# Kernel optimization log

Hardware: AMD Instinct MI355X
Metric: run time of the kernel (lower is better)

Reference implementation:

```python
import jax, jax.numpy as jnp
import numpy as np

B, H, W, D, C = 2, 128, 128, 8, 64
HEADS, DIM_HEAD = 4, 16
F_IN = C * D            # 512
F_OUT = DIM_HEAD * HEADS * D  # 512


def setup_inputs() -> dict:
    key = jax.random.key(0)
    ks = jax.random.split(key, 8)
    s = 0.02
    return {
        "x_in": jax.random.normal(ks[0], (B, H, W, D, C), dtype=jnp.float32),
        "Wq": jax.random.normal(ks[1], (F_IN, F_OUT), dtype=jnp.float32) * s,
        "Wk": jax.random.normal(ks[2], (F_IN, F_OUT), dtype=jnp.float32) * s,
        "Wv": jax.random.normal(ks[3], (F_IN, F_OUT), dtype=jnp.float32) * s,
        "rescale": jnp.ones((HEADS, 1, 1), dtype=jnp.float32),
        "Wp": jax.random.normal(ks[4], (F_OUT, F_IN), dtype=jnp.float32) * s,
        "bp": jnp.zeros((F_IN,), dtype=jnp.float32),
        "pos_w1": jax.random.normal(ks[5], (C, 1, 3, 3, 3), dtype=jnp.float32) * s,
        "pos_w2": jax.random.normal(ks[6], (C, 1, 3, 3, 3), dtype=jnp.float32) * s,
    }


def _dwconv3d(y, kern, groups):
    # y: [b,c,d,h,w], kern: [c,1,3,3,3] depthwise
    return jax.lax.conv_general_dilated(
        y, kern, window_strides=(1, 1, 1), padding="SAME",
        feature_group_count=groups,
        dimension_numbers=("NCDHW", "OIDHW", "NCDHW"))


def reference(x_in, Wq, Wk, Wv, rescale, Wp, bp, pos_w1, pos_w2):
    b, h, w, d, c = x_in.shape
    heads = rescale.shape[0]
    n = h * w
    x = x_in.reshape(b, n, d * c)
    q_inp = x @ Wq
    k_inp = x @ Wk
    v_inp = x @ Wv

    def split(t):  # [b,n,heads*Dh] -> [b,heads,Dh,n]  (Dh = dim_head*num_frm)
        return t.reshape(b, n, heads, -1).transpose(0, 2, 3, 1)

    q, k, v = split(q_inp), split(k_inp), split(v_inp)
    # L2-normalize along spatial axis n (last dim), torch F.normalize eps=1e-12
    q = q / jnp.maximum(jnp.linalg.norm(q, axis=-1, keepdims=True), 1e-12)
    k = k / jnp.maximum(jnp.linalg.norm(k, axis=-1, keepdims=True), 1e-12)
    # channel attention: [b,heads,Dh,Dh]
    attn = jnp.einsum("bhdn,bhen->bhde", k, q) * rescale
    attn = jax.nn.softmax(attn, axis=-1)
    out = jnp.einsum("bhde,bhen->bhdn", attn, v)  # [b,heads,Dh,n]
    out = out.transpose(0, 3, 1, 2).reshape(b, n, -1)  # [b,n,heads*Dh]
    out_c = (out @ Wp + bp).reshape(b, h, w, d, c)

    # positional branch: depthwise conv3d over [b,c,d,h,w]
    vp = v_inp.reshape(b, h, w, d, c).transpose(0, 4, 3, 1, 2)
    p = _dwconv3d(vp, pos_w1, c)
    p = jax.nn.gelu(p, approximate=False)
    p = _dwconv3d(p, pos_w2, c)
    out_p = p.transpose(0, 3, 4, 2, 1)  # -> [b,h,w,d,c]
    return out_c + out_p
```

## Files before the change

### kernel.cpp

```cpp
#include <hip/hip_runtime.h>
#include <math.h>
#include <stdint.h>


using short8  = __attribute__((ext_vector_type(8))) short;
using short4v = __attribute__((ext_vector_type(4))) short;
using f32x4   = __attribute__((ext_vector_type(4))) float;

__device__ __forceinline__ float bf2f(unsigned short u) {
  union { unsigned int i; float f; } v; v.i = ((unsigned int)u) << 16; return v.f;
}
__device__ __forceinline__ unsigned short f2bf(float f) {
  union { float f; unsigned int i; } v; v.f = f;
  unsigned int r = v.i + 0x7fffu + ((v.i >> 16) & 1u);
  return (unsigned short)(r >> 16);
}

__device__ __forceinline__ void g2l16(const void* g, void* l) {
  __builtin_amdgcn_global_load_lds(
      (__attribute__((address_space(1))) void*)(unsigned long long)(uintptr_t)g,
      (__attribute__((address_space(3))) void*)(unsigned int)(uintptr_t)l,
      16, 0, 0);
}

__global__ __launch_bounds__(256) void convert_x(const float* __restrict__ x,
                                                 unsigned short* __restrict__ xb) {
  int i = (blockIdx.x * 256 + threadIdx.x) * 4;
  float4 v = *(const float4*)&x[i];
  ushort4 o;
  o.x = f2bf(v.x); o.y = f2bf(v.y); o.z = f2bf(v.z); o.w = f2bf(v.w);
  *(ushort4*)&xb[i] = o;
}

__global__ __launch_bounds__(256) void prep_w(const float* __restrict__ Wq,
                                              const float* __restrict__ Wk,
                                              const float* __restrict__ Wv,
                                              const float* __restrict__ Wp,
                                              unsigned short* __restrict__ Wcat_t,
                                              unsigned short* __restrict__ Wp_t) {
  __shared__ unsigned short Ls[32 * 36];
  int bid = blockIdx.x;
  int mat = bid >> 8, tile = bid & 255;
  int tr = (tile >> 4) * 32, tc = (tile & 15) * 32;
  const float* src = (mat == 0) ? Wq : (mat == 1) ? Wk : (mat == 2) ? Wv : Wp;
  int t = threadIdx.x;
  int r = t >> 3, c4 = (t & 7) * 4;
  float4 v = *(const float4*)&src[(tr + r) * 512 + tc + c4];
  Ls[(c4 + 0) * 36 + r] = f2bf(v.x);
  Ls[(c4 + 1) * 36 + r] = f2bf(v.y);
  Ls[(c4 + 2) * 36 + r] = f2bf(v.z);
  Ls[(c4 + 3) * 36 + r] = f2bf(v.w);
  __syncthreads();
  int rn = t >> 3, ck4 = (t & 7) * 4;
  ushort4 o;
  o.x = Ls[rn * 36 + ck4 + 0]; o.y = Ls[rn * 36 + ck4 + 1];
  o.z = Ls[rn * 36 + ck4 + 2]; o.w = Ls[rn * 36 + ck4 + 3];
  unsigned short* dst = (mat < 3)
      ? &Wcat_t[(long)(mat * 512 + tc + rn) * 512 + tr + ck4]
      : &Wp_t[(long)(tc + rn) * 512 + tr + ck4];
  *(ushort4*)dst = o;
}

__global__ __launch_bounds__(256) void gemm_lds(
    const unsigned short* __restrict__ A, const unsigned short* __restrict__ Bt,
    unsigned short* __restrict__ C, const float* __restrict__ bias,
    int lda, int ldb, int ldc, int K, long sA, long sB, long sC) {
  __shared__ unsigned short As[128 * 64];
  __shared__ unsigned short Bs[128 * 64];
  const int t = threadIdx.x;
  const int n0 = blockIdx.x * 128, m0 = blockIdx.y * 128;
  A  += (long)blockIdx.z * sA + (long)m0 * lda;
  Bt += (long)blockIdx.z * sB + (long)n0 * ldb;
  C  += (long)blockIdx.z * sC;
  const int lane = t & 63, w = t >> 6;
  const int wm = w >> 1, wn = w & 1;
  const int quad = lane >> 4, l16 = lane & 15;
  const int sr = lane >> 3;
  const int sc = lane & 7;

  f32x4 acc[4][4] = {};

  for (int k0 = 0; k0 < K; k0 += 64) {
#pragma unroll
    for (int q = 0; q < 4; q++) {
      int r = q * 32 + w * 8 + sr;
      int ca = (sc ^ sr) * 8;
      g2l16(&A[(long)r * lda + k0 + ca], &As[(q * 32 + w * 8) * 64]);
      g2l16(&Bt[(long)r * ldb + k0 + ca], &Bs[(q * 32 + w * 8) * 64]);
    }
    __syncthreads();
#pragma unroll
    for (int kk = 0; kk < 2; kk++) {
      short8 af[4], bfq[4];
#pragma unroll
      for (int i = 0; i < 4; i++) {
        int r = wm * 64 + i * 16 + l16;
        int s = (kk * 4 + quad) ^ (r & 7);
        af[i] = *(const short8*)&As[r * 64 + s * 8];
      }
#pragma unroll
      for (int j = 0; j < 4; j++) {
        int r = wn * 64 + j * 16 + l16;
        int s = (kk * 4 + quad) ^ (r & 7);
        bfq[j] = *(const short8*)&Bs[r * 64 + s * 8];
      }
#pragma unroll
      for (int i = 0; i < 4; i++)
#pragma unroll
        for (int j = 0; j < 4; j++)
          acc[i][j] = __builtin_amdgcn_mfma_f32_16x16x32_bf16(bfq[j], af[i], acc[i][j], 0, 0, 0);
    }
    __syncthreads();
  }

#pragma unroll
  for (int i = 0; i < 4; i++) {
    long rbase = (long)(m0 + wm * 64 + i * 16 + l16) * ldc;
#pragma unroll
    for (int j = 0; j < 4; j++) {
      int col = n0 + wn * 64 + j * 16 + quad * 4;
      float b0 = 0.f, b1 = 0.f, b2 = 0.f, b3 = 0.f;
      if (bias) { float4 bv = *(const float4*)&bias[col]; b0 = bv.x; b1 = bv.y; b2 = bv.z; b3 = bv.w; }
      uint2 o;
      o.x = (unsigned)f2bf(acc[i][j][0] + b0) | ((unsigned)f2bf(acc[i][j][1] + b1) << 16);
      o.y = (unsigned)f2bf(acc[i][j][2] + b2) | ((unsigned)f2bf(acc[i][j][3] + b3) << 16);
      *(uint2*)&C[rbase + col] = o;
    }
  }
}

__global__ __launch_bounds__(256) void gram_kernel(const unsigned short* __restrict__ qkv,
                                                   float* __restrict__ Gp,
                                                   float* __restrict__ ss) {
  __shared__ unsigned short Qs[128 * 36];
  __shared__ unsigned short Ks[128 * 36];
  int ns = blockIdx.x, h = blockIdx.y, b = blockIdx.z;
  int t = threadIdx.x;
  const int lane = t & 63, wave = t >> 6;
  const int wm = wave >> 1, wn = wave & 1;
  const int quad = lane >> 4, l16 = lane & 15;
  long base = (long)b * 16384 * 1536;
  int m = t >> 7;
  int tt = t & 127;
  int cg = tt & 31;
  int rg = tt >> 5;
  int colb = (m ? (512 + h * 128) : (h * 128)) + cg * 4;
  unsigned short* dst = m ? Ks : Qs;

  f32x4 acc[4][4] = {};
  float ssp[4] = {0.f, 0.f, 0.f, 0.f};

  for (int s = 0; s < 16; s++) {
    int n0 = ns * 512 + s * 32;
    unsigned short sv[8][4];
#pragma unroll
    for (int rr = 0; rr < 8; rr++) {
      int n = n0 + rg * 8 + rr;
      uint2 v = *(const uint2*)&qkv[base + (long)n * 1536 + colb];
      sv[rr][0] = (unsigned short)(v.x & 0xffff);
      sv[rr][1] = (unsigned short)(v.x >> 16);
      sv[rr][2] = (unsigned short)(v.y & 0xffff);
      sv[rr][3] = (unsigned short)(v.y >> 16);
    }
#pragma unroll
    for (int rr = 0; rr < 8; rr++)
#pragma unroll
      for (int j = 0; j < 4; j++) {
        float fv = bf2f(sv[rr][j]);
        ssp[j] += fv * fv;
      }
#pragma unroll
    for (int j = 0; j < 4; j++) {
      int col = cg * 4 + j;
      ushort4 w0 = { sv[0][j], sv[1][j], sv[2][j], sv[3][j] };
      ushort4 w1 = { sv[4][j], sv[5][j], sv[6][j], sv[7][j] };
      *(ushort4*)&dst[col * 36 + rg * 8]     = w0;
      *(ushort4*)&dst[col * 36 + rg * 8 + 4] = w1;
    }
    __syncthreads();
    short8 af[4], bfq[4];
#pragma unroll
    for (int i = 0; i < 4; i++) {
      const unsigned short* p = &Ks[(wm * 64 + i * 16 + l16) * 36 + quad * 8];
      union { short8 v8; short4v v4[2]; } u;
      u.v4[0] = *(const short4v*)p; u.v4[1] = *(const short4v*)(p + 4);
      af[i] = u.v8;
    }
#pragma unroll
    for (int j = 0; j < 4; j++) {
      const unsigned short* p = &Qs[(wn * 64 + j * 16 + l16) * 36 + quad * 8];
      union { short8 v8; short4v v4[2]; } u;
      u.v4[0] = *(const short4v*)p; u.v4[1] = *(const short4v*)(p + 4);
      bfq[j] = u.v8;
    }
#pragma unroll
    for (int i = 0; i < 4; i++)
#pragma unroll
      for (int j = 0; j < 4; j++)
        acc[i][j] = __builtin_amdgcn_mfma_f32_16x16x32_bf16(bfq[j], af[i], acc[i][j], 0, 0, 0);
    __syncthreads();
  }

  float* gp = Gp + ((long)ns * 8 + b * 4 + h) * 16384;
#pragma unroll
  for (int i = 0; i < 4; i++) {
    int row = wm * 64 + i * 16 + l16;
#pragma unroll
    for (int j = 0; j < 4; j++) {
      int col = wn * 64 + j * 16 + quad * 4;
      *(f32x4*)&gp[row * 128 + col] = acc[i][j];
    }
  }

  float* sred = (float*)Qs;
#pragma unroll
  for (int j = 0; j < 4; j++) sred[(m * 128 + cg * 4 + j) * 5 + rg] = ssp[j];
  __syncthreads();
  {
    float s = sred[t * 5 + 0] + sred[t * 5 + 1] + sred[t * 5 + 2] + sred[t * 5 + 3];
    int m2 = t >> 7, col = t & 127;
    atomicAdd(&ss[b * 1024 + m2 * 512 + h * 128 + col], s);
  }
}

__global__ __launch_bounds__(256) void reduce_g(const float* __restrict__ Gp,
                                                float* __restrict__ G) {
  int i = blockIdx.x * 256 + threadIdx.x;
  float s = 0.f;
#pragma unroll 8
  for (int ns = 0; ns < 32; ns++) s += Gp[(long)ns * 131072 + i];
  G[i] = s;
}

__global__ __launch_bounds__(256) void softmax_kernel(const float* __restrict__ G,
                                                      const float* __restrict__ ss,
                                                      const float* __restrict__ rescale,
                                                      unsigned short* __restrict__ Abd) {
  __shared__ float L[128 * 129];
  __shared__ float rsq[128];
  __shared__ float rsk[128];
  int h = blockIdx.x, b = blockIdx.y;
  int t = threadIdx.x;
  const float* g = G + (long)(b * 4 + h) * 16384;
  if (t < 128) rsq[t] = rsqrtf(fmaxf(ss[b * 1024 + h * 128 + t], 1e-24f));
  else { int d = t - 128; rsk[d] = rsqrtf(fmaxf(ss[b * 1024 + 512 + h * 128 + d], 1e-24f)); }
  __syncthreads();
  float rs = rescale[h];
  for (int i = t; i < 16384; i += 256) {
    int d = i >> 7, e = i & 127;
    L[d * 129 + e] = g[i] * rsk[d] * rsq[e] * rs;
  }
  __syncthreads();
  if (t < 128) {
    float* row = &L[t * 129];
    float mx = -1e30f;
    for (int e = 0; e < 128; e++) mx = fmaxf(mx, row[e]);
    float sum = 0.0f;
    for (int e = 0; e < 128; e++) { float ex = __expf(row[e] - mx); row[e] = ex; sum += ex; }
    float inv = 1.0f / sum;
    long abase = (long)b * 262144;
    for (int e = 0; e < 128; e++)
      Abd[abase + (long)(h * 128 + e) * 512 + h * 128 + t] = f2bf(row[e] * inv);
  }
}

template <bool GELU, bool ADD>
__global__ __launch_bounds__(256) void dwconv_kernel(
    const unsigned short* __restrict__ in, int inld,
    const float* __restrict__ wgt,
    const unsigned short* __restrict__ addc,
    unsigned short* __restrict__ outb,
    float* __restrict__ outf) {
  __shared__ unsigned short tile[100 * 512];
  __shared__ float wl[27 * 64];
  int wt = blockIdx.x, ht = blockIdx.y, b = blockIdx.z;
  int t = threadIdx.x;
  for (int i = t; i < 1728; i += 256) {
    int c = i / 27, tap = i % 27;
    wl[tap * 64 + c] = wgt[i];
  }
  int h0 = ht * 8, w0 = wt * 8;
  int lg = t & 63;
#pragma unroll 5
  for (int rr = 0; rr < 25; rr++) {
    int row = rr * 4 + (t >> 6);
    int hh = row / 10, ww = row % 10;
    int gh = h0 + hh - 1, gw = w0 + ww - 1;
    uint4 v = {0u, 0u, 0u, 0u};
    if ((unsigned)gh < 128u && (unsigned)gw < 128u)
      v = *(const uint4*)&in[(long)(b * 16384 + gh * 128 + gw) * inld + lg * 8];
    *(uint4*)&tile[row * 512 + lg * 8] = v;
  }
  __syncthreads();

  int f0 = lg * 8;
  int d = f0 >> 6, c0 = f0 & 63;
  int pg = t >> 6;
  for (int P = 0; P < 4; P++) {
    float acc[4][8] = {};
    for (int kd = 0; kd < 3; kd++) {
      int dz = d + kd - 1;
      if ((unsigned)dz >= 8u) continue;
      int fz = dz * 64 + c0;
#pragma unroll
      for (int kh = 0; kh < 3; kh++)
#pragma unroll
        for (int kw = 0; kw < 3; kw++) {
          int tap = kd * 9 + kh * 3 + kw;
          float w[8];
          *(float4*)&w[0] = *(const float4*)&wl[tap * 64 + c0];
          *(float4*)&w[4] = *(const float4*)&wl[tap * 64 + c0 + 4];
#pragma unroll
          for (int s = 0; s < 4; s++) {
            int pos = P * 16 + pg * 4 + s;
            int ph = pos >> 3, pw = pos & 7;
            uint4 pv = *(const uint4*)&tile[((ph + kh) * 10 + pw + kw) * 512 + fz];
            const unsigned short* u = (const unsigned short*)&pv;
#pragma unroll
            for (int j = 0; j < 8; j++) acc[s][j] += bf2f(u[j]) * w[j];
          }
        }
    }
    for (int s = 0; s < 4; s++) {
      int pos = P * 16 + pg * 4 + s;
      int ph = pos >> 3, pw = pos & 7;
      long row = (long)(b * 16384 + (h0 + ph) * 128 + (w0 + pw));
      if (GELU) {
        unsigned short o[8];
#pragma unroll
        for (int j = 0; j < 8; j++) {
          float x = acc[s][j];
          o[j] = f2bf(0.5f * x * (1.0f + erff(x * 0.70710678118654752f)));
        }
        *(uint4*)&outb[row * 512 + f0] = *(uint4*)&o[0];
      } else {
        uint4 av = *(const uint4*)&addc[row * 512 + f0];
        const unsigned short* au = (const unsigned short*)&av;
        float o[8];
#pragma unroll
        for (int j = 0; j < 8; j++) o[j] = acc[s][j] + bf2f(au[j]);
        *(float4*)&outf[row * 512 + f0]     = *(float4*)&o[0];
        *(float4*)&outf[row * 512 + f0 + 4] = *(float4*)&o[4];
      }
    }
  }
}

extern "C" void kernel_launch(void* const* d_in, const int* in_sizes, int n_in,
                              void* d_out, int out_size, void* d_ws, size_t ws_size,
                              hipStream_t stream) {
  const float* x   = (const float*)d_in[0];
  const float* Wq  = (const float*)d_in[1];
  const float* Wk  = (const float*)d_in[2];
  const float* Wv  = (const float*)d_in[3];
  const float* rsc = (const float*)d_in[4];
  const float* Wp  = (const float*)d_in[5];
  const float* bp  = (const float*)d_in[6];
  const float* pw1 = (const float*)d_in[7];
  const float* pw2 = (const float*)d_in[8];
  float* out = (float*)d_out;

  char* ws = (char*)d_ws;
  unsigned short* x_bf   = (unsigned short*)(ws + 0);
  unsigned short* qkv    = (unsigned short*)(ws + 33554432);
  unsigned short* Wcat_t = (unsigned short*)(ws + 134217728);
  unsigned short* Wp_t   = (unsigned short*)(ws + 135790592);
  float*          ss     = (float*)(ws + 136314880);
  float*          G      = (float*)(ws + 136323072);
  unsigned short* Abd    = (unsigned short*)(ws + 136847360);
  unsigned short* Mt     = (unsigned short*)(ws + 137895936);
  unsigned short* out_c  = (unsigned short*)(ws + 138944512);
  float*          Gp     = (float*)(ws + 0);
  unsigned short* p1     = x_bf;

  hipMemsetAsync(ss, 0, 8192, stream);
  hipMemsetAsync(Abd, 0, 1048576, stream);

  convert_x<<<16384, 256, 0, stream>>>(x, x_bf);
  prep_w<<<1024, 256, 0, stream>>>(Wq, Wk, Wv, Wp, Wcat_t, Wp_t);

  gemm_lds<<<dim3(12, 256, 1), 256, 0, stream>>>(
      x_bf, Wcat_t, qkv, nullptr, 512, 512, 1536, 512, 0L, 0L, 0L);

  gram_kernel<<<dim3(32, 4, 2), 256, 0, stream>>>(qkv, Gp, ss);
  reduce_g<<<512, 256, 0, stream>>>(Gp, G);
  softmax_kernel<<<dim3(4, 2, 1), 256, 0, stream>>>(G, ss, rsc, Abd);

  gemm_lds<<<dim3(4, 4, 2), 256, 0, stream>>>(
      Wp_t, Abd, Mt, nullptr, 512, 512, 512, 512, 0L, 262144L, 262144L);

  gemm_lds<<<dim3(4, 128, 2), 256, 0, stream>>>(
      qkv + 1024, Mt, out_c, bp, 1536, 512, 512, 512,
      (long)16384 * 1536, 262144L, (long)16384 * 512);

  dwconv_kernel<true, false><<<dim3(16, 16, 2), 256, 0, stream>>>(
      qkv + 1024, 1536, pw1, nullptr, p1, nullptr);
  dwconv_kernel<false, true><<<dim3(16, 16, 2), 256, 0, stream>>>(
      p1, 512, pw2, out_c, nullptr, out);
}
```

Measured before the change: 409.6 us.

## Fuse Q/K projection with per-tile Gram computation and shrink dwconv tiles

Replaces the QKV GEMM plus separate Gram kernel with one fused kernel. For Q and K, each block computes a 128-row projection tile, transposes it in LDS, and immediately forms a partial Gram matrix and squared norms, so Q and K are never written to global memory. Only V is stored, as a compact 512-wide buffer. The reduce step now sums 128 partial Gram tiles per batch instead of 32, which writes and reads far more partial data. The depthwise conv uses 4x8 tiles with row-register reuse across kw, trading a larger halo fraction for more blocks and fewer LDS reads.

```diff
diff --git a/kernel.cpp b/kernel.cpp
--- a/kernel.cpp
+++ b/kernel.cpp
@@ -4,7 +4,6 @@
 
 
 using short8  = __attribute__((ext_vector_type(8))) short;
-using short4v = __attribute__((ext_vector_type(4))) short;
 using f32x4   = __attribute__((ext_vector_type(4))) float;
 
 __device__ __forceinline__ float bf2f(unsigned short u) {
@@ -61,6 +60,219 @@
   *(ushort4*)dst = o;
 }
 
+__global__ __launch_bounds__(256, 2) void fused_qkv(
+    const unsigned short* __restrict__ x_bf,
+    const unsigned short* __restrict__ Wcat_t,
+    unsigned short* __restrict__ v,
+    float* __restrict__ Gp, float* __restrict__ ss) {
+  __shared__ unsigned short sh[38912];
+  unsigned short* As = sh;
+  unsigned short* B0 = sh + 8192;
+  unsigned short* B1 = sh + 16384;
+  const int job = blockIdx.x, mt = blockIdx.y, b = blockIdx.z;
+  const int t = threadIdx.x;
+  const int lane = t & 63, w = t >> 6;
+  const int wm = w >> 1, wn = w & 1;
+  const int quad = lane >> 4, l16 = lane & 15;
+  const int sr = lane >> 3, sc = lane & 7;
+  const unsigned short* A = x_bf + ((long)b * 16384 + mt * 128) * 512;
+
+  if (job >= 4) {
+    const unsigned short* Bt = Wcat_t + (long)(1024 + (job - 4) * 128) * 512;
+    f32x4 acc[4][4] = {};
+    for (int k0 = 0; k0 < 512; k0 += 64) {
+#pragma unroll
+      for (int q = 0; q < 4; q++) {
+        int r = q * 32 + w * 8 + sr;
+        int ca = (sc ^ sr) * 8;
+        g2l16(&A[(long)r * 512 + k0 + ca], &As[(q * 32 + w * 8) * 64]);
+        g2l16(&Bt[(long)r * 512 + k0 + ca], &B0[(q * 32 + w * 8) * 64]);
+      }
+      __syncthreads();
+#pragma unroll
+      for (int kk = 0; kk < 2; kk++) {
+        short8 af[4], bf[4];
+#pragma unroll
+        for (int i = 0; i < 4; i++) {
+          int r = wm * 64 + i * 16 + l16;
+          int s = (kk * 4 + quad) ^ (r & 7);
+          af[i] = *(const short8*)&As[r * 64 + s * 8];
+        }
+#pragma unroll
+        for (int j = 0; j < 4; j++) {
+          int r = wn * 64 + j * 16 + l16;
+          int s = (kk * 4 + quad) ^ (r & 7);
+          bf[j] = *(const short8*)&B0[r * 64 + s * 8];
+        }
+#pragma unroll
+        for (int i = 0; i < 4; i++)
+#pragma unroll
+          for (int j = 0; j < 4; j++)
+            acc[i][j] = __builtin_amdgcn_mfma_f32_16x16x32_bf16(bf[j], af[i], acc[i][j], 0, 0, 0);
+      }
+      __syncthreads();
+    }
+    unsigned short* vout = v + ((long)b * 16384 + mt * 128) * 512 + (job - 4) * 128;
+#pragma unroll
+    for (int i = 0; i < 4; i++) {
+      long rbase = (long)(wm * 64 + i * 16 + l16) * 512;
+#pragma unroll
+      for (int j = 0; j < 4; j++) {
+        int col = wn * 64 + j * 16 + quad * 4;
+        uint2 o;
+        o.x = (unsigned)f2bf(acc[i][j][0]) | ((unsigned)f2bf(acc[i][j][1]) << 16);
+        o.y = (unsigned)f2bf(acc[i][j][2]) | ((unsigned)f2bf(acc[i][j][3]) << 16);
+        *(uint2*)&vout[rbase + col] = o;
+      }
+    }
+  } else {
+    const int h = job;
+    const unsigned short* Bq = Wcat_t + (long)(h * 128) * 512;
+    const unsigned short* Bk = Wcat_t + (long)(512 + h * 128) * 512;
+    f32x4 aq[4][4] = {}, ak[4][4] = {};
+    for (int k0 = 0; k0 < 512; k0 += 64) {
+#pragma unroll
+      for (int q = 0; q < 4; q++) {
+        int r = q * 32 + w * 8 + sr;
+        int ca = (sc ^ sr) * 8;
+        g2l16(&A[(long)r * 512 + k0 + ca],  &As[(q * 32 + w * 8) * 64]);
+        g2l16(&Bq[(long)r * 512 + k0 + ca], &B0[(q * 32 + w * 8) * 64]);
+        g2l16(&Bk[(long)r * 512 + k0 + ca], &B1[(q * 32 + w * 8) * 64]);
+      }
+      __syncthreads();
+#pragma unroll
+      for (int kk = 0; kk < 2; kk++) {
+        short8 af[4], bq[4], bk[4];
+#pragma unroll
+        for (int i = 0; i < 4; i++) {
+          int r = wm * 64 + i * 16 + l16;
+          int s = (kk * 4 + quad) ^ (r & 7);
+          af[i] = *(const short8*)&As[r * 64 + s * 8];
+        }
+#pragma unroll
+        for (int j = 0; j < 4; j++) {
+          int r = wn * 64 + j * 16 + l16;
+          int s = (kk * 4 + quad) ^ (r & 7);
+          bq[j] = *(const short8*)&B0[r * 64 + s * 8];
+          bk[j] = *(const short8*)&B1[r * 64 + s * 8];
+        }
+#pragma unroll
+        for (int i = 0; i < 4; i++)
+#pragma unroll
+          for (int j = 0; j < 4; j++) {
+            aq[i][j] = __builtin_amdgcn_mfma_f32_16x16x32_bf16(af[i], bq[j], aq[i][j], 0, 0, 0);
+            ak[i][j] = __builtin_amdgcn_mfma_f32_16x16x32_bf16(af[i], bk[j], ak[i][j], 0, 0, 0);
+          }
+      }
+      __syncthreads();
+    }
+    unsigned short* kT = sh;
+    unsigned short* qT = sh + 17408;
+    float* red = (float*)(sh + 34816);
+#pragma unroll
+    for (int i = 0; i < 4; i++) {
+      int mm = wm * 64 + i * 16 + quad * 4;
+#pragma unroll
+      for (int j = 0; j < 4; j++) {
+        int f = wn * 64 + j * 16 + l16;
+        ushort4 oq = { f2bf(aq[i][j][0]), f2bf(aq[i][j][1]), f2bf(aq[i][j][2]), f2bf(aq[i][j][3]) };
+        ushort4 ok = { f2bf(ak[i][j][0]), f2bf(ak[i][j][1]), f2bf(ak[i][j][2]), f2bf(ak[i][j][3]) };
+        *(ushort4*)&qT[f * 136 + mm] = oq;
+        *(ushort4*)&kT[f * 136 + mm] = ok;
+      }
+    }
+    int grp = wm * 4 + quad;
+#pragma unroll
+    for (int j = 0; j < 4; j++) {
+      float pq = 0.f, pk = 0.f;
+#pragma unroll
+      for (int i = 0; i < 4; i++)
+#pragma unroll
+        for (int r = 0; r < 4; r++) { pq += aq[i][j][r] * aq[i][j][r]; pk += ak[i][j][r] * ak[i][j][r]; }
+      int col = wn * 64 + j * 16 + l16;
+      red[grp * 128 + col] = pq;
+      red[1024 + grp * 128 + col] = pk;
+    }
+    __syncthreads();
+    f32x4 g[4][4] = {};
+#pragma unroll
+    for (int kk2 = 0; kk2 < 4; kk2++) {
+      short8 afk[4], bfq[4];
+#pragma unroll
+      for (int i = 0; i < 4; i++)
+        afk[i] = *(const short8*)&kT[(wm * 64 + i * 16 + l16) * 136 + kk2 * 32 + quad * 8];
+#pragma unroll
+      for (int j = 0; j < 4; j++)
+        bfq[j] = *(const short8*)&qT[(wn * 64 + j * 16 + l16) * 136 + kk2 * 32 + quad * 8];
+#pragma unroll
+      for (int i = 0; i < 4; i++)
+#pragma unroll
+        for (int j = 0; j < 4; j++)
+          g[i][j] = __builtin_amdgcn_mfma_f32_16x16x32_bf16(afk[i], bfq[j], g[i][j], 0, 0, 0);
+    }
+    float* gp = Gp + (((long)(b * 128 + mt) * 4 + h) << 14);
+#pragma unroll
+    for (int i = 0; i < 4; i++) {
+      int dd = wm * 64 + i * 16 + quad * 4;
+#pragma unroll
+      for (int j = 0; j < 4; j++) {
+        int e = wn * 64 + j * 16 + l16;
+        *(f32x4*)&gp[e * 128 + dd] = g[i][j];
+      }
+    }
+    {
+      int sel = t >> 7, col = t & 127;
+      float s = 0.f;
+#pragma unroll
+      for (int g2 = 0; g2 < 8; g2++) s += red[sel * 1024 + g2 * 128 + col];
+      atomicAdd(&ss[b * 1024 + sel * 512 + h * 128 + col], s);
+    }
+  }
+}
+
+__global__ __launch_bounds__(256) void reduce_g(const float* __restrict__ Gp,
+                                                float* __restrict__ G) {
+  int i = blockIdx.x * 256 + threadIdx.x;
+  int b = i >> 16, h = (i >> 14) & 3, r = i & 16383;
+  const float* p = Gp + (((long)b * 512 + h) << 14) + r;
+  float s = 0.f;
+#pragma unroll 8
+  for (int mtv = 0; mtv < 128; mtv++) s += p[(long)mtv * 65536];
+  G[i] = s;
+}
+
+__global__ __launch_bounds__(256) void softmax_kernel(const float* __restrict__ Gt,
+                                                      const float* __restrict__ ss,
+                                                      const float* __restrict__ rescale,
+                                                      unsigned short* __restrict__ Abd) {
+  __shared__ float L[128 * 129];
+  __shared__ float rsq[128];
+  __shared__ float rsk[128];
+  int h = blockIdx.x, b = blockIdx.y;
+  int t = threadIdx.x;
+  const float* g = Gt + (long)(b * 4 + h) * 16384;
+  if (t < 128) rsq[t] = rsqrtf(fmaxf(ss[b * 1024 + h * 128 + t], 1e-24f));
+  else { int d = t - 128; rsk[d] = rsqrtf(fmaxf(ss[b * 1024 + 512 + h * 128 + d], 1e-24f)); }
+  __syncthreads();
+  float rs = rescale[h];
+  for (int i = t; i < 16384; i += 256) {
+    int e = i >> 7, d = i & 127;
+    L[d * 129 + e] = g[i] * rsk[d] * rsq[e] * rs;
+  }
+  __syncthreads();
+  if (t < 128) {
+    float* row = &L[t * 129];
+    float mx = -1e30f;
+    for (int e = 0; e < 128; e++) mx = fmaxf(mx, row[e]);
+    float sum = 0.0f;
+    for (int e = 0; e < 128; e++) { float ex = __expf(row[e] - mx); row[e] = ex; sum += ex; }
+    float inv = 1.0f / sum;
+    long abase = (long)b * 262144;
+    for (int e = 0; e < 128; e++)
+      Abd[abase + (long)(h * 128 + e) * 512 + h * 128 + t] = f2bf(row[e] * inv);
+  }
+}
+
 __global__ __launch_bounds__(256) void gemm_lds(
     const unsigned short* __restrict__ A, const unsigned short* __restrict__ Bt,
     unsigned short* __restrict__ C, const float* __restrict__ bias,
@@ -75,8 +287,7 @@
   const int lane = t & 63, w = t >> 6;
   const int wm = w >> 1, wn = w & 1;
   const int quad = lane >> 4, l16 = lane & 15;
-  const int sr = lane >> 3;
-  const int sc = lane & 7;
+  const int sr = lane >> 3, sc = lane & 7;
 
   f32x4 acc[4][4] = {};
 
@@ -129,149 +340,14 @@
   }
 }
 
-__global__ __launch_bounds__(256) void gram_kernel(const unsigned short* __restrict__ qkv,
-                                                   float* __restrict__ Gp,
-                                                   float* __restrict__ ss) {
-  __shared__ unsigned short Qs[128 * 36];
-  __shared__ unsigned short Ks[128 * 36];
-  int ns = blockIdx.x, h = blockIdx.y, b = blockIdx.z;
-  int t = threadIdx.x;
-  const int lane = t & 63, wave = t >> 6;
-  const int wm = wave >> 1, wn = wave & 1;
-  const int quad = lane >> 4, l16 = lane & 15;
-  long base = (long)b * 16384 * 1536;
-  int m = t >> 7;
-  int tt = t & 127;
-  int cg = tt & 31;
-  int rg = tt >> 5;
-  int colb = (m ? (512 + h * 128) : (h * 128)) + cg * 4;
-  unsigned short* dst = m ? Ks : Qs;
-
-  f32x4 acc[4][4] = {};
-  float ssp[4] = {0.f, 0.f, 0.f, 0.f};
-
-  for (int s = 0; s < 16; s++) {
-    int n0 = ns * 512 + s * 32;
-    unsigned short sv[8][4];
-#pragma unroll
-    for (int rr = 0; rr < 8; rr++) {
-      int n = n0 + rg * 8 + rr;
-      uint2 v = *(const uint2*)&qkv[base + (long)n * 1536 + colb];
-      sv[rr][0] = (unsigned short)(v.x & 0xffff);
-      sv[rr][1] = (unsigned short)(v.x >> 16);
-      sv[rr][2] = (unsigned short)(v.y & 0xffff);
-      sv[rr][3] = (unsigned short)(v.y >> 16);
-    }
-#pragma unroll
-    for (int rr = 0; rr < 8; rr++)
-#pragma unroll
-      for (int j = 0; j < 4; j++) {
-        float fv = bf2f(sv[rr][j]);
-        ssp[j] += fv * fv;
-      }
-#pragma unroll
-    for (int j = 0; j < 4; j++) {
-      int col = cg * 4 + j;
-      ushort4 w0 = { sv[0][j], sv[1][j], sv[2][j], sv[3][j] };
-      ushort4 w1 = { sv[4][j], sv[5][j], sv[6][j], sv[7][j] };
-      *(ushort4*)&dst[col * 36 + rg * 8]     = w0;
-      *(ushort4*)&dst[col * 36 + rg * 8 + 4] = w1;
-    }
-    __syncthreads();
-    short8 af[4], bfq[4];
-#pragma unroll
-    for (int i = 0; i < 4; i++) {
-      const unsigned short* p = &Ks[(wm * 64 + i * 16 + l16) * 36 + quad * 8];
-      union { short8 v8; short4v v4[2]; } u;
-      u.v4[0] = *(const short4v*)p; u.v4[1] = *(const short4v*)(p + 4);
-      af[i] = u.v8;
-    }
-#pragma unroll
-    for (int j = 0; j < 4; j++) {
-      const unsigned short* p = &Qs[(wn * 64 + j * 16 + l16) * 36 + quad * 8];
-      union { short8 v8; short4v v4[2]; } u;
-      u.v4[0] = *(const short4v*)p; u.v4[1] = *(const short4v*)(p + 4);
-      bfq[j] = u.v8;
-    }
-#pragma unroll
-    for (int i = 0; i < 4; i++)
-#pragma unroll
-      for (int j = 0; j < 4; j++)
-        acc[i][j] = __builtin_amdgcn_mfma_f32_16x16x32_bf16(bfq[j], af[i], acc[i][j], 0, 0, 0);
-    __syncthreads();
-  }
-
-  float* gp = Gp + ((long)ns * 8 + b * 4 + h) * 16384;
-#pragma unroll
-  for (int i = 0; i < 4; i++) {
-    int row = wm * 64 + i * 16 + l16;
-#pragma unroll
-    for (int j = 0; j < 4; j++) {
-      int col = wn * 64 + j * 16 + quad * 4;
-      *(f32x4*)&gp[row * 128 + col] = acc[i][j];
-    }
-  }
-
-  float* sred = (float*)Qs;
-#pragma unroll
-  for (int j = 0; j < 4; j++) sred[(m * 128 + cg * 4 + j) * 5 + rg] = ssp[j];
-  __syncthreads();
-  {
-    float s = sred[t * 5 + 0] + sred[t * 5 + 1] + sred[t * 5 + 2] + sred[t * 5 + 3];
-    int m2 = t >> 7, col = t & 127;
-    atomicAdd(&ss[b * 1024 + m2 * 512 + h * 128 + col], s);
-  }
-}
-
-__global__ __launch_bounds__(256) void reduce_g(const float* __restrict__ Gp,
-                                                float* __restrict__ G) {
-  int i = blockIdx.x * 256 + threadIdx.x;
-  float s = 0.f;
-#pragma unroll 8
-  for (int ns = 0; ns < 32; ns++) s += Gp[(long)ns * 131072 + i];
-  G[i] = s;
-}
-
-__global__ __launch_bounds__(256) void softmax_kernel(const float* __restrict__ G,
-                                                      const float* __restrict__ ss,
-                                                      const float* __restrict__ rescale,
-                                                      unsigned short* __restrict__ Abd) {
-  __shared__ float L[128 * 129];
-  __shared__ float rsq[128];
-  __shared__ float rsk[128];
-  int h = blockIdx.x, b = blockIdx.y;
-  int t = threadIdx.x;
-  const float* g = G + (long)(b * 4 + h) * 16384;
-  if (t < 128) rsq[t] = rsqrtf(fmaxf(ss[b * 1024 + h * 128 + t], 1e-24f));
-  else { int d = t - 128; rsk[d] = rsqrtf(fmaxf(ss[b * 1024 + 512 + h * 128 + d], 1e-24f)); }
-  __syncthreads();
-  float rs = rescale[h];
-  for (int i = t; i < 16384; i += 256) {
-    int d = i >> 7, e = i & 127;
-    L[d * 129 + e] = g[i] * rsk[d] * rsq[e] * rs;
-  }
-  __syncthreads();
-  if (t < 128) {
-    float* row = &L[t * 129];
-    float mx = -1e30f;
-    for (int e = 0; e < 128; e++) mx = fmaxf(mx, row[e]);
-    float sum = 0.0f;
-    for (int e = 0; e < 128; e++) { float ex = __expf(row[e] - mx); row[e] = ex; sum += ex; }
-    float inv = 1.0f / sum;
-    long abase = (long)b * 262144;
-    for (int e = 0; e < 128; e++)
-      Abd[abase + (long)(h * 128 + e) * 512 + h * 128 + t] = f2bf(row[e] * inv);
-  }
-}
-
-template <bool GELU, bool ADD>
+template <bool GELU>
 __global__ __launch_bounds__(256) void dwconv_kernel(
-    const unsigned short* __restrict__ in, int inld,
+    const unsigned short* __restrict__ in,
     const float* __restrict__ wgt,
     const unsigned short* __restrict__ addc,
     unsigned short* __restrict__ outb,
     float* __restrict__ outf) {
-  __shared__ unsigned short tile[100 * 512];
+  __shared__ unsigned short tile[60 * 512];
   __shared__ float wl[27 * 64];
   int wt = blockIdx.x, ht = blockIdx.y, b = blockIdx.z;
   int t = threadIdx.x;
@@ -279,58 +355,65 @@
     int c = i / 27, tap = i % 27;
     wl[tap * 64 + c] = wgt[i];
   }
-  int h0 = ht * 8, w0 = wt * 8;
+  int h0 = ht * 4, w0 = wt * 8;
   int lg = t & 63;
 #pragma unroll 5
-  for (int rr = 0; rr < 25; rr++) {
+  for (int rr = 0; rr < 15; rr++) {
     int row = rr * 4 + (t >> 6);
     int hh = row / 10, ww = row % 10;
     int gh = h0 + hh - 1, gw = w0 + ww - 1;
-    uint4 v = {0u, 0u, 0u, 0u};
+    uint4 vv = {0u, 0u, 0u, 0u};
     if ((unsigned)gh < 128u && (unsigned)gw < 128u)
-      v = *(const uint4*)&in[(long)(b * 16384 + gh * 128 + gw) * inld + lg * 8];
-    *(uint4*)&tile[row * 512 + lg * 8] = v;
+      vv = *(const uint4*)&in[((long)(b * 16384 + gh * 128 + gw)) * 512 + lg * 8];
+    *(uint4*)&tile[row * 512 + lg * 8] = vv;
   }
   __syncthreads();
 
   int f0 = lg * 8;
   int d = f0 >> 6, c0 = f0 & 63;
   int pg = t >> 6;
-  for (int P = 0; P < 4; P++) {
+  int pwb = (pg & 1) * 4;
+#pragma unroll
+  for (int P = 0; P < 2; P++) {
+    int ph = P * 2 + (pg >> 1);
     float acc[4][8] = {};
     for (int kd = 0; kd < 3; kd++) {
       int dz = d + kd - 1;
       if ((unsigned)dz >= 8u) continue;
       int fz = dz * 64 + c0;
 #pragma unroll
-      for (int kh = 0; kh < 3; kh++)
+      for (int kh = 0; kh < 3; kh++) {
+        float tf[6][8];
+#pragma unroll
+        for (int cc = 0; cc < 6; cc++) {
+          uint4 pv = *(const uint4*)&tile[((ph + kh) * 10 + pwb + cc) * 512 + fz];
+          const unsigned short* u = (const unsigned short*)&pv;
+#pragma unroll
+          for (int j = 0; j < 8; j++) tf[cc][j] = bf2f(u[j]);
+        }
 #pragma unroll
         for (int kw = 0; kw < 3; kw++) {
           int tap = kd * 9 + kh * 3 + kw;
-          float w[8];
-          *(float4*)&w[0] = *(const float4*)&wl[tap * 64 + c0];
-          *(float4*)&w[4] = *(const float4*)&wl[tap * 64 + c0 + 4];
-#pragma unroll
-          for (int s = 0; s < 4; s++) {
-            int pos = P * 16 + pg * 4 + s;
-            int ph = pos >> 3, pw = pos & 7;
-            uint4 pv = *(const uint4*)&tile[((ph + kh) * 10 + pw + kw) * 512 + fz];
-            const unsigned short* u = (const unsigned short*)&pv;
-#pragma unroll
-            for (int j = 0; j < 8; j++) acc[s][j] += bf2f(u[j]) * w[j];
-          }
-        }
-    }
+          float wv[8];
+          *(float4*)&wv[0] = *(const float4*)&wl[tap * 64 + c0];
+          *(float4*)&wv[4] = *(const float4*)&wl[tap * 64 + c0 + 4];
+#pragma unroll
+          for (int s = 0; s < 4; s++)
+#pragma unroll
+            for (int j = 0; j < 8; j++) acc[s][j] += tf[s + kw][j] * wv[j];
+        }
+      }
+    }
+#pragma unroll
     for (int s = 0; s < 4; s++) {
-      int pos = P * 16 + pg * 4 + s;
-      int ph = pos >> 3, pw = pos & 7;
+      int pw = pwb + s;
       long row = (long)(b * 16384 + (h0 + ph) * 128 + (w0 + pw));
       if (GELU) {
         unsigned short o[8];
 #pragma unroll
         for (int j = 0; j < 8; j++) {
-          float x = acc[s][j];
-          o[j] = f2bf(0.5f * x * (1.0f + erff(x * 0.70710678118654752f)));
+          float xg = acc[s][j];
+          o[j] = f2bf(0.5f * xg * (1.0f + erff(xg * 0.70710678118654752f)));
         }
         *(uint4*)&outb[row * 512 + f0] = *(uint4*)&o[0];
       } else {
@@ -362,15 +445,15 @@
 
   char* ws = (char*)d_ws;
   unsigned short* x_bf   = (unsigned short*)(ws + 0);
-  unsigned short* qkv    = (unsigned short*)(ws + 33554432);
-  unsigned short* Wcat_t = (unsigned short*)(ws + 134217728);
-  unsigned short* Wp_t   = (unsigned short*)(ws + 135790592);
-  float*          ss     = (float*)(ws + 136314880);
-  float*          G      = (float*)(ws + 136323072);
-  unsigned short* Abd    = (unsigned short*)(ws + 136847360);
-  unsigned short* Mt     = (unsigned short*)(ws + 137895936);
-  unsigned short* out_c  = (unsigned short*)(ws + 138944512);
-  float*          Gp     = (float*)(ws + 0);
+  unsigned short* v      = (unsigned short*)(ws + 33554432);
+  unsigned short* out_c  = (unsigned short*)(ws + 67108864);
+  float*          Gp     = (float*)(ws + 100663296);
+  unsigned short* Wcat_t = (unsigned short*)(ws + 167772160);
+  unsigned short* Wp_t   = (unsigned short*)(ws + 169345024);
+  float*          ss     = (float*)(ws + 169869312);
+  float*          G      = (float*)(ws + 169877504);
+  unsigned short* Abd    = (unsigned short*)(ws + 170401792);
+  unsigned short* Mt     = (unsigned short*)(ws + 171450368);
   unsigned short* p1     = x_bf;
 
   hipMemsetAsync(ss, 0, 8192, stream);
@@ -379,10 +462,7 @@
   convert_x<<<16384, 256, 0, stream>>>(x, x_bf);
   prep_w<<<1024, 256, 0, stream>>>(Wq, Wk, Wv, Wp, Wcat_t, Wp_t);
 
-  gemm_lds<<<dim3(12, 256, 1), 256, 0, stream>>>(
-      x_bf, Wcat_t, qkv, nullptr, 512, 512, 1536, 512, 0L, 0L, 0L);
-
-  gram_kernel<<<dim3(32, 4, 2), 256, 0, stream>>>(qkv, Gp, ss);
+  fused_qkv<<<dim3(8, 128, 2), 256, 0, stream>>>(x_bf, Wcat_t, v, Gp, ss);
   reduce_g<<<512, 256, 0, stream>>>(Gp, G);
   softmax_kernel<<<dim3(4, 2, 1), 256, 0, stream>>>(G, ss, rsc, Abd);
 
@@ -390,11 +470,11 @@
       Wp_t, Abd, Mt, nullptr, 512, 512, 512, 512, 0L, 262144L, 262144L);
 
   gemm_lds<<<dim3(4, 128, 2), 256, 0, stream>>>(
-      qkv + 1024, Mt, out_c, bp, 1536, 512, 512, 512,
-      (long)16384 * 1536, 262144L, (long)16384 * 512);
-
-  dwconv_kernel<true, false><<<dim3(16, 16, 2), 256, 0, stream>>>(
-      qkv + 1024, 1536, pw1, nullptr, p1, nullptr);
-  dwconv_kernel<false, true><<<dim3(16, 16, 2), 256, 0, stream>>>(
-      p1, 512, pw2, out_c, nullptr, out);
-}
+      v, Mt, out_c, bp, 512, 512, 512, 512,
+      (long)16384 * 512, 262144L, (long)16384 * 512);
+
+  dwconv_kernel<true><<<dim3(16, 32, 2), 256, 0, stream>>>(
+      v, pw1, nullptr, p1, nullptr);
+  dwconv_kernel<false><<<dim3(16, 32, 2), 256, 0, stream>>>(
+      p1, pw2, out_c, nullptr, out);
+}
```

After: 383.9 us. 1.07x faster.
